# Kernel optimization log

Measured on AMD Instinct MI355X. Metric: run time of the kernel, lower is better.

## Reference

```python
import jax, jax.numpy as jnp
import numpy as np

N = 100000   # nodes
E = 1000000  # directed edges
C = 64       # channels
K = 4        # propagation hops
DT = 1.0     # dt; exp_init=False branch: 2*x + dt^2*conv(x) - x_pre


def setup_inputs() -> dict:
    key = jax.random.key(0)
    k1, k2, k3, k4, k5 = jax.random.split(key, 5)
    x = jax.random.normal(k1, (N, C), dtype=jnp.float32)
    x_pre = jax.random.normal(k2, (N, C), dtype=jnp.float32)
    edge_index = jax.random.randint(k3, (2, E), 0, N, dtype=jnp.int32)
    bound = 1.0 / np.sqrt(C)  # PyG Linear default (kaiming-uniform-like)
    W = jax.random.uniform(k4, (C, C), jnp.float32, -bound, bound)
    b = jax.random.uniform(k5, (C,), jnp.float32, -bound, bound)
    return {"x": x, "x_pre": x_pre, "edge_index": edge_index, "W": W, "b": b}


def _sgc(x, edge_index, W, b):
    # gcn_norm: add self-loops, symmetric normalization D^-1/2 (A+I) D^-1/2
    loop = jnp.arange(N, dtype=edge_index.dtype)
    src = jnp.concatenate([edge_index[0], loop])  # source j
    dst = jnp.concatenate([edge_index[1], loop])  # target i
    deg = jax.ops.segment_sum(jnp.ones(src.shape, jnp.float32), dst, num_segments=N)
    dinv = jnp.where(deg > 0, jax.lax.rsqrt(deg), 0.0)
    norm = dinv[src] * dinv[dst]  # [E+N]
    h = x
    for _ in range(K):  # K-hop sparse propagation (gather -> scale -> scatter-add)
        h = jax.ops.segment_sum(h[src] * norm[:, None], dst, num_segments=N)
    return h @ W.T + b  # SGConv final linear


def reference(x, x_pre, edge_index, W, b):
    return 2.0 * x + (DT * DT) * _sgc(x, edge_index, W, b) - x_pre
```

## Files before the change

### kernel.cpp

```cpp
#include <hip/hip_runtime.h>
#include <hip/hip_fp16.h>

#define CCH 64
#define NBLK 128
#define BKT  256


__global__ void countA(const int* __restrict__ dst, int* __restrict__ cntmat,
                       int E, int chunk, int B) {
    __shared__ int h[512];
    int t = threadIdx.x, blk = blockIdx.x;
    for (int i = t; i < B; i += 256) h[i] = 0;
    __syncthreads();
    int e0 = blk * chunk, e1 = min(e0 + chunk, E);
    for (int e = e0 + t; e < e1; e += 256) atomicAdd(&h[dst[e] >> 8], 1);
    __syncthreads();
    for (int i = t; i < B; i += 256) cntmat[i * NBLK + blk] = h[i];
}

__global__ void scan1(const int* __restrict__ cnt, int* __restrict__ part,
                      int* __restrict__ bsum, int N) {
    __shared__ int s[256];
    int t = threadIdx.x;
    int base = blockIdx.x * 1024 + t * 4;
    int v0 = (base + 0 < N) ? cnt[base + 0] : 0;
    int v1 = (base + 1 < N) ? cnt[base + 1] : 0;
    int v2 = (base + 2 < N) ? cnt[base + 2] : 0;
    int v3 = (base + 3 < N) ? cnt[base + 3] : 0;
    s[t] = v0 + v1 + v2 + v3;
    __syncthreads();
    for (int off = 1; off < 256; off <<= 1) {
        int xx = (t >= off) ? s[t - off] : 0;
        __syncthreads();
        s[t] += xx;
        __syncthreads();
    }
    int excl = (t == 0) ? 0 : s[t - 1];
    if (t == 255) bsum[blockIdx.x] = s[255];
    if (base + 0 < N) part[base + 0] = excl;
    if (base + 1 < N) part[base + 1] = excl + v0;
    if (base + 2 < N) part[base + 2] = excl + v0 + v1;
    if (base + 3 < N) part[base + 3] = excl + v0 + v1 + v2;
}

__global__ void scan2(int* __restrict__ bsum, int NB) {
    __shared__ int s[256];
    int t = threadIdx.x;
    int base = t * 4;
    int v0 = (base + 0 < NB) ? bsum[base + 0] : 0;
    int v1 = (base + 1 < NB) ? bsum[base + 1] : 0;
    int v2 = (base + 2 < NB) ? bsum[base + 2] : 0;
    int v3 = (base + 3 < NB) ? bsum[base + 3] : 0;
    s[t] = v0 + v1 + v2 + v3;
    __syncthreads();
    for (int off = 1; off < 256; off <<= 1) {
        int xx = (t >= off) ? s[t - off] : 0;
        __syncthreads();
        s[t] += xx;
        __syncthreads();
    }
    int excl = (t == 0) ? 0 : s[t - 1];
    if (base + 0 < NB) bsum[base + 0] = excl;
    if (base + 1 < NB) bsum[base + 1] = excl + v0;
    if (base + 2 < NB) bsum[base + 2] = excl + v0 + v1;
    if (base + 3 < NB) bsum[base + 3] = excl + v0 + v1 + v2;
}

__global__ void partA(const int* __restrict__ src, const int* __restrict__ dst,
                      const int* __restrict__ part, const int* __restrict__ bsum,
                      unsigned* __restrict__ brec, int E, int chunk, int B) {
    __shared__ int cur[512];
    int t = threadIdx.x, blk = blockIdx.x;
    for (int i = t; i < B; i += 256) {
        int idx = i * NBLK + blk;
        cur[i] = part[idx] + bsum[idx >> 10];
    }
    __syncthreads();
    int e0 = blk * chunk, e1 = min(e0 + chunk, E);
    for (int e = e0 + t; e < e1; e += 256) {
        int s = src[e], d = dst[e];
        int pos = atomicAdd(&cur[d >> 8], 1);
        brec[pos] = ((unsigned)s << 8) | (unsigned)(d & 255);
    }
}

__global__ void buildB(const unsigned* __restrict__ brec, const int* __restrict__ part,
                       const int* __restrict__ bsum, int* __restrict__ row_ptr,
                       int* __restrict__ adj, float* __restrict__ dinv,
                       float* __restrict__ dinv2, const float* __restrict__ x,
                       __half* __restrict__ xh, int N, int B, int E) {
    __shared__ int hist[256];
    __shared__ int scanbuf[256];
    __shared__ int cursor[256];
    __shared__ float sdinv[256];
    int t = threadIdx.x, k = blockIdx.x;
    int i0 = k * NBLK;
    int base = part[i0] + bsum[i0 >> 10];
    int nextb;
    if (k + 1 < B) {
        int i1 = (k + 1) * NBLK;
        nextb = part[i1] + bsum[i1 >> 10];
    } else {
        nextb = E;
    }
    hist[t] = 0;
    __syncthreads();
    for (int i = base + t; i < nextb; i += 256) atomicAdd(&hist[brec[i] & 255u], 1);
    __syncthreads();
    int v = hist[t];
    scanbuf[t] = v;
    __syncthreads();
    for (int o = 1; o < 256; o <<= 1) {
        int xx = (t >= o) ? scanbuf[t - o] : 0;
        __syncthreads();
        scanbuf[t] += xx;
        __syncthreads();
    }
    int excl = scanbuf[t] - v;
    int node = k * 256 + t;
    float di = 0.f;
    if (node < N) {
        int p = base + excl;
        row_ptr[node] = p;
        cursor[t] = p;
        float dp1 = (float)v + 1.0f;
        di = rsqrtf(dp1);
        dinv[node]  = di;
        dinv2[node] = 1.0f / dp1;
    }
    sdinv[t] = di;
    if (k == 0 && t == 0) row_ptr[N] = E;
    __syncthreads();
    for (int i = base + t; i < nextb; i += 256) {
        unsigned r = brec[i];
        int pos = atomicAdd(&cursor[r & 255u], 1);
        adj[pos] = (int)(r >> 8);
    }
    int nodeBase = k * 256;
    for (int i = t; i < 2048; i += 256) {
        int nl = i >> 3;
        int node2 = nodeBase + nl;
        if (node2 < N) {
            float d = sdinv[nl];
            size_t baseE = (size_t)node2 * 64 + (size_t)(i & 7) * 8;
            float4 a = *(const float4*)&x[baseE];
            float4 c = *(const float4*)&x[baseE + 4];
            float4 o;
            __half2* op = (__half2*)&o;
            op[0] = __float22half2_rn(make_float2(d * a.x, d * a.y));
            op[1] = __float22half2_rn(make_float2(d * a.z, d * a.w));
            op[2] = __float22half2_rn(make_float2(d * c.x, d * c.y));
            op[3] = __float22half2_rn(make_float2(d * c.z, d * c.w));
            *(float4*)&xh[baseE] = o;
        }
    }
}


__device__ __forceinline__ void acc16w(float4 hv, float w, float* acc) {
    __half2* hp = (__half2*)&hv;
    #pragma unroll
    for (int i2 = 0; i2 < 4; ++i2) {
        float2 f = __half22float2(hp[i2]);
        acc[2 * i2]     = fmaf(w, f.x, acc[2 * i2]);
        acc[2 * i2 + 1] = fmaf(w, f.y, acc[2 * i2 + 1]);
    }
}

__global__ void __launch_bounds__(256, 8)
prop_kernel(const __half* __restrict__ hin, __half* __restrict__ hout,
            const int* __restrict__ row_ptr, const int* __restrict__ adj,
            const float* __restrict__ scale, int N, int E) {
    int wid  = (blockIdx.x * blockDim.x + threadIdx.x) >> 6;
    int lane = threadIdx.x & 63;
    int g    = lane >> 3;
    int q    = lane & 7;
    int g8   = g << 3;
    int nb   = wid << 3;
    if (nb >= N) return;
    int node  = nb + g;
    int nodeC = (node < N) ? node : (N - 1);
    int rp0 = row_ptr[nodeC];
    int rp1 = row_ptr[nodeC + 1];
    int cnt = (node < N) ? (rp1 - rp0) : 0;

    int R = cnt;
    R = max(R, __shfl_xor(R, 8, 64));
    R = max(R, __shfl_xor(R, 16, 64));
    R = max(R, __shfl_xor(R, 32, 64));

    const float4* hin16 = (const float4*)hin;

    int eCur = adj[rp0 + q];
    int eNxt = adj[rp0 + 8 + q];

    float4 selfv = hin16[(size_t)nodeC * 8 + q];

    int j0 = __shfl(eCur, g8 + 0, 64); j0 = (0 < cnt) ? j0 : 0;
    int j1 = __shfl(eCur, g8 + 1, 64); j1 = (1 < cnt) ? j1 : 0;
    int j2 = __shfl(eCur, g8 + 2, 64); j2 = (2 < cnt) ? j2 : 0;
    int j3 = __shfl(eCur, g8 + 3, 64); j3 = (3 < cnt) ? j3 : 0;
    float4 gA0 = hin16[(size_t)j0 * 8 + q];
    float4 gA1 = hin16[(size_t)j1 * 8 + q];
    float4 gA2 = hin16[(size_t)j2 * 8 + q];
    float4 gA3 = hin16[(size_t)j3 * 8 + q];
    float4 gB0, gB1, gB2, gB3;

    float acc[8] = {0.f, 0.f, 0.f, 0.f, 0.f, 0.f, 0.f, 0.f};
    acc16w(selfv, 1.f, acc);

    for (int r = 0; r < R; r += 8) {
        int t;
        t = r + 4; j0 = __shfl(eCur, g8 + (t & 7), 64); j0 = (t < cnt) ? j0 : 0;
        t = r + 5; j1 = __shfl(eCur, g8 + (t & 7), 64); j1 = (t < cnt) ? j1 : 0;
        t = r + 6; j2 = __shfl(eCur, g8 + (t & 7), 64); j2 = (t < cnt) ? j2 : 0;
        t = r + 7; j3 = __shfl(eCur, g8 + (t & 7), 64); j3 = (t < cnt) ? j3 : 0;
        gB0 = hin16[(size_t)j0 * 8 + q];
        gB1 = hin16[(size_t)j1 * 8 + q];
        gB2 = hin16[(size_t)j2 * 8 + q];
        gB3 = hin16[(size_t)j3 * 8 + q];
        float w;
        w = (r + 0 < cnt) ? 1.f : 0.f; acc16w(gA0, w, acc);
        w = (r + 1 < cnt) ? 1.f : 0.f; acc16w(gA1, w, acc);
        w = (r + 2 < cnt) ? 1.f : 0.f; acc16w(gA2, w, acc);
        w = (r + 3 < cnt) ? 1.f : 0.f; acc16w(gA3, w, acc);
        t = r + 8;  j0 = __shfl(eNxt, g8 + (t & 7), 64); j0 = (t < cnt) ? j0 : 0;
        t = r + 9;  j1 = __shfl(eNxt, g8 + (t & 7), 64); j1 = (t < cnt) ? j1 : 0;
        t = r + 10; j2 = __shfl(eNxt, g8 + (t & 7), 64); j2 = (t < cnt) ? j2 : 0;
        t = r + 11; j3 = __shfl(eNxt, g8 + (t & 7), 64); j3 = (t < cnt) ? j3 : 0;
        gA0 = hin16[(size_t)j0 * 8 + q];
        gA1 = hin16[(size_t)j1 * 8 + q];
        gA2 = hin16[(size_t)j2 * 8 + q];
        gA3 = hin16[(size_t)j3 * 8 + q];
        w = (r + 4 < cnt) ? 1.f : 0.f; acc16w(gB0, w, acc);
        w = (r + 5 < cnt) ? 1.f : 0.f; acc16w(gB1, w, acc);
        w = (r + 6 < cnt) ? 1.f : 0.f; acc16w(gB2, w, acc);
        w = (r + 7 < cnt) ? 1.f : 0.f; acc16w(gB3, w, acc);
        eCur = eNxt;
        int ao = rp0 + r + 16;
        ao = (ao > E + 96) ? (E + 96) : ao;
        eNxt = adj[ao + q];
    }

    float sc = scale[nodeC];
    if (node < N) {
        float4 o;
        __half2* op = (__half2*)&o;
        op[0] = __float22half2_rn(make_float2(sc * acc[0], sc * acc[1]));
        op[1] = __float22half2_rn(make_float2(sc * acc[2], sc * acc[3]));
        op[2] = __float22half2_rn(make_float2(sc * acc[4], sc * acc[5]));
        op[3] = __float22half2_rn(make_float2(sc * acc[6], sc * acc[7]));
        ((float4*)hout)[(size_t)node * 8 + q] = o;
    }
}

__global__ void __launch_bounds__(256, 2)
final_kernel(const __half* __restrict__ h, const float* __restrict__ x,
             const float* __restrict__ xp, const float* __restrict__ W,
             const float* __restrict__ b, float* __restrict__ out, int N) {
    __shared__ __align__(16) float ht[64 * 68];
    __shared__ __align__(16) float Wt[64 * 68];
    int t = threadIdx.x;
    int nodeBase = blockIdx.x * 64;

    for (int i = t; i < 1024; i += 256) {
        int c  = i >> 4;
        int k4 = i & 15;
        float4 w4 = ((const float4*)W)[i];
        Wt[(k4 * 4 + 0) * 68 + c] = w4.x;
        Wt[(k4 * 4 + 1) * 68 + c] = w4.y;
        Wt[(k4 * 4 + 2) * 68 + c] = w4.z;
        Wt[(k4 * 4 + 3) * 68 + c] = w4.w;
    }
    for (int i = t; i < 512; i += 256) {
        int n  = i >> 3;
        int k8 = i & 7;
        int node = nodeBase + n;
        float4 hv = (node < N) ? ((const float4*)h)[node * 8 + k8]
                               : make_float4(0.f, 0.f, 0.f, 0.f);
        __half2* hp = (__half2*)&hv;
        #pragma unroll
        for (int j = 0; j < 4; ++j) {
            float2 f = __half22float2(hp[j]);
            ht[(k8 * 8 + 2 * j)     * 68 + n] = f.x;
            ht[(k8 * 8 + 2 * j + 1) * 68 + n] = f.y;
        }
    }
    __syncthreads();

    int r0 = (t >> 4) * 4;
    int c0 = (t & 15) * 4;
    float acc[4][4] = {};
    #pragma unroll 8
    for (int k = 0; k < 64; ++k) {
        float4 hv = *(const float4*)&ht[k * 68 + r0];
        float4 wv = *(const float4*)&Wt[k * 68 + c0];
        acc[0][0] = fmaf(hv.x, wv.x, acc[0][0]);
        acc[0][1] = fmaf(hv.x, wv.y, acc[0][1]);
        acc[0][2] = fmaf(hv.x, wv.z, acc[0][2]);
        acc[0][3] = fmaf(hv.x, wv.w, acc[0][3]);
        acc[1][0] = fmaf(hv.y, wv.x, acc[1][0]);
        acc[1][1] = fmaf(hv.y, wv.y, acc[1][1]);
        acc[1][2] = fmaf(hv.y, wv.z, acc[1][2]);
        acc[1][3] = fmaf(hv.y, wv.w, acc[1][3]);
        acc[2][0] = fmaf(hv.z, wv.x, acc[2][0]);
        acc[2][1] = fmaf(hv.z, wv.y, acc[2][1]);
        acc[2][2] = fmaf(hv.z, wv.z, acc[2][2]);
        acc[2][3] = fmaf(hv.z, wv.w, acc[2][3]);
        acc[3][0] = fmaf(hv.w, wv.x, acc[3][0]);
        acc[3][1] = fmaf(hv.w, wv.y, acc[3][1]);
        acc[3][2] = fmaf(hv.w, wv.z, acc[3][2]);
        acc[3][3] = fmaf(hv.w, wv.w, acc[3][3]);
    }

    float4 bv = *(const float4*)&b[c0];
    #pragma unroll
    for (int i = 0; i < 4; ++i) {
        int node = nodeBase + r0 + i;
        if (node >= N) continue;
        int base = node * 64 + c0;
        float4 xv = *(const float4*)&x[base];
        float4 pv = *(const float4*)&xp[base];
        float4 o;
        o.x = fmaf(2.f, xv.x, acc[i][0] + bv.x) - pv.x;
        o.y = fmaf(2.f, xv.y, acc[i][1] + bv.y) - pv.y;
        o.z = fmaf(2.f, xv.z, acc[i][2] + bv.z) - pv.z;
        o.w = fmaf(2.f, xv.w, acc[i][3] + bv.w) - pv.w;
        *(float4*)&out[base] = o;
    }
}

extern "C" void kernel_launch(void* const* d_in, const int* in_sizes, int n_in,
                              void* d_out, int out_size, void* d_ws, size_t ws_size,
                              hipStream_t stream) {
    const float* x    = (const float*)d_in[0];
    const float* xpre = (const float*)d_in[1];
    const int*   ei   = (const int*)d_in[2];
    const float* W    = (const float*)d_in[3];
    const float* b    = (const float*)d_in[4];
    float* out = (float*)d_out;

    const int N = in_sizes[0] / CCH;
    const int E = in_sizes[2] / 2;
    const int* src = ei;
    const int* dst = ei + E;

    const int B     = (N + BKT - 1) / BKT;
    const int M     = B * NBLK;
    const int chunk = (E + NBLK - 1) / NBLK;
    const int NB2   = (M + 1023) / 1024;

    char* p = (char*)d_ws;
    auto alloc = [&](size_t bytes) -> char* {
        char* r = p;
        p += (bytes + 255) & ~(size_t)255;
        return r;
    };
    int*      cntmat  = (int*)alloc((size_t)M * 4);
    int*      part    = (int*)alloc((size_t)M * 4);
    int*      bsum    = (int*)alloc((size_t)NB2 * 4);
    unsigned* brec    = (unsigned*)alloc((size_t)E * 4);
    int*      adj     = (int*)alloc(((size_t)E + 128) * 4);
    int*      row_ptr = (int*)alloc(((size_t)N + 1) * 4);
    float*    dinv    = (float*)alloc((size_t)N * 4);
    float*    dinv2   = (float*)alloc((size_t)N * 4);
    __half*   xh      = (__half*)alloc((size_t)N * CCH * 2);
    __half*   g0      = (__half*)alloc((size_t)N * CCH * 2);
    __half*   g1      = (__half*)alloc((size_t)N * CCH * 2);

    countA<<<NBLK, 256, 0, stream>>>(dst, cntmat, E, chunk, B);
    scan1 <<<NB2, 256, 0, stream>>>(cntmat, part, bsum, M);
    scan2 <<<1, 256, 0, stream>>>(bsum, NB2);
    partA <<<NBLK, 256, 0, stream>>>(src, dst, part, bsum, brec, E, chunk, B);
    buildB<<<B, 256, 0, stream>>>(brec, part, bsum, row_ptr, adj, dinv, dinv2,
                                  x, xh, N, B, E);

    const int nwave = (N + 7) / 8;
    const int pgrid = (nwave + 3) / 4;
    prop_kernel<<<pgrid, 256, 0, stream>>>(xh, g0, row_ptr, adj, dinv2, N, E);
    prop_kernel<<<pgrid, 256, 0, stream>>>(g0, g1, row_ptr, adj, dinv2, N, E);
    prop_kernel<<<pgrid, 256, 0, stream>>>(g1, g0, row_ptr, adj, dinv2, N, E);
    prop_kernel<<<pgrid, 256, 0, stream>>>(g0, g1, row_ptr, adj, dinv,  N, E);

    final_kernel<<<(N + 63) / 64, 256, 0, stream>>>(g1, x, xpre, W, b, out, N);
}
```

Measured before the change: 264.9 us.

## Sort nodes by degree so each wave processes similar-degree nodes

Builds a global in-degree histogram in buildB, scans it, and scatters node ids into a degree-sorted permutation. prop_kernel then maps its 8 nodes per wavefront through that permutation, so the per-wave loop bound (max degree in the group) sits close to each node's real degree and fewer masked gather slots are wasted. The gather loop also skips the B and next-A batches when they fall past the wave's max degree. This adds two small kernels and an extra indirection per node, and it breaks the locality of output writes and self-feature reads, which now follow the permutation instead of node order.

```diff
diff --git a/kernel.cpp b/kernel.cpp
--- a/kernel.cpp
+++ b/kernel.cpp
@@ -4,12 +4,14 @@
 #define CCH 64
 #define NBLK 128
 #define BKT  256
+#define PB   64
 
 
 __global__ void countA(const int* __restrict__ dst, int* __restrict__ cntmat,
-                       int E, int chunk, int B) {
+                       int* __restrict__ ghist, int E, int chunk, int B) {
     __shared__ int h[512];
     int t = threadIdx.x, blk = blockIdx.x;
+    if (blk == 0) ghist[t] = 0;
     for (int i = t; i < B; i += 256) h[i] = 0;
     __syncthreads();
     int e0 = blk * chunk, e1 = min(e0 + chunk, E);
@@ -88,10 +90,12 @@
                        const int* __restrict__ bsum, int* __restrict__ row_ptr,
                        int* __restrict__ adj, float* __restrict__ dinv,
                        float* __restrict__ dinv2, const float* __restrict__ x,
-                       __half* __restrict__ xh, int N, int B, int E) {
+                       __half* __restrict__ xh, int* __restrict__ ghist,
+                       int N, int B, int E) {
     __shared__ int hist[256];
     __shared__ int scanbuf[256];
     __shared__ int cursor[256];
+    __shared__ int dh[256];
     __shared__ float sdinv[256];
     int t = threadIdx.x, k = blockIdx.x;
     int i0 = k * NBLK;
@@ -104,6 +108,7 @@
         nextb = E;
     }
     hist[t] = 0;
+    dh[t] = 0;
     __syncthreads();
     for (int i = base + t; i < nextb; i += 256) atomicAdd(&hist[brec[i] & 255u], 1);
     __syncthreads();
@@ -127,10 +132,12 @@
         di = rsqrtf(dp1);
         dinv[node]  = di;
         dinv2[node] = 1.0f / dp1;
+        atomicAdd(&dh[v < 255 ? v : 255], 1);
     }
     sdinv[t] = di;
     if (k == 0 && t == 0) row_ptr[N] = E;
     __syncthreads();
+    if (dh[t]) atomicAdd(&ghist[t], dh[t]);
     for (int i = base + t; i < nextb; i += 256) {
         unsigned r = brec[i];
         int pos = atomicAdd(&cursor[r & 255u], 1);
@@ -156,6 +163,44 @@
     }
 }
 
+__global__ void permScan(int* __restrict__ h) {
+    __shared__ int s[256];
+    int t = threadIdx.x;
+    int v = h[t];
+    s[t] = v;
+    __syncthreads();
+    for (int o = 1; o < 256; o <<= 1) {
+        int xx = (t >= o) ? s[t - o] : 0;
+        __syncthreads();
+        s[t] += xx;
+        __syncthreads();
+    }
+    h[t] = s[t] - v;
+}
+
+__global__ void permScatter(const int* __restrict__ row_ptr, int* __restrict__ goff,
+                            int* __restrict__ perm, int N, int chunk) {
+    __shared__ int h[256];
+    __shared__ int cur[256];
+    int t = threadIdx.x, blk = blockIdx.x;
+    h[t] = 0;
+    __syncthreads();
+    int n0 = blk * chunk, n1 = min(n0 + chunk, N);
+    for (int n = n0 + t; n < n1; n += 256) {
+        int d = row_ptr[n + 1] - row_ptr[n];
+        atomicAdd(&h[d < 255 ? d : 255], 1);
+    }
+    __syncthreads();
+    if (h[t]) cur[t] = atomicAdd(&goff[t], h[t]);
+    __syncthreads();
+    for (int n = n0 + t; n < n1; n += 256) {
+        int d = row_ptr[n + 1] - row_ptr[n];
+        d = d < 255 ? d : 255;
+        int pos = atomicAdd(&cur[d], 1);
+        perm[pos] = n;
+    }
+}
+
 
 __device__ __forceinline__ void acc16w(float4 hv, float w, float* acc) {
     __half2* hp = (__half2*)&hv;
@@ -170,7 +215,8 @@
 __global__ void __launch_bounds__(256, 8)
 prop_kernel(const __half* __restrict__ hin, __half* __restrict__ hout,
             const int* __restrict__ row_ptr, const int* __restrict__ adj,
-            const float* __restrict__ scale, int N, int E) {
+            const float* __restrict__ scale, const int* __restrict__ perm,
+            int N, int E) {
     int wid  = (blockIdx.x * blockDim.x + threadIdx.x) >> 6;
     int lane = threadIdx.x & 63;
     int g    = lane >> 3;
@@ -178,11 +224,12 @@
     int g8   = g << 3;
     int nb   = wid << 3;
     if (nb >= N) return;
-    int node  = nb + g;
-    int nodeC = (node < N) ? node : (N - 1);
-    int rp0 = row_ptr[nodeC];
-    int rp1 = row_ptr[nodeC + 1];
-    int cnt = (node < N) ? (rp1 - rp0) : 0;
+    int  slot  = nb + g;
+    bool valid = slot < N;
+    int  node  = perm[valid ? slot : 0];
+    int rp0 = row_ptr[node];
+    int rp1 = row_ptr[node + 1];
+    int cnt = valid ? (rp1 - rp0) : 0;
 
     int R = cnt;
     R = max(R, __shfl_xor(R, 8, 64));
@@ -190,60 +237,72 @@
     R = max(R, __shfl_xor(R, 32, 64));
 
     const float4* hin16 = (const float4*)hin;
+    float4 selfv = hin16[(size_t)node * 8 + q];
 
     int eCur = adj[rp0 + q];
-    int eNxt = adj[rp0 + 8 + q];
-
-    float4 selfv = hin16[(size_t)nodeC * 8 + q];
-
-    int j0 = __shfl(eCur, g8 + 0, 64); j0 = (0 < cnt) ? j0 : 0;
-    int j1 = __shfl(eCur, g8 + 1, 64); j1 = (1 < cnt) ? j1 : 0;
-    int j2 = __shfl(eCur, g8 + 2, 64); j2 = (2 < cnt) ? j2 : 0;
-    int j3 = __shfl(eCur, g8 + 3, 64); j3 = (3 < cnt) ? j3 : 0;
-    float4 gA0 = hin16[(size_t)j0 * 8 + q];
-    float4 gA1 = hin16[(size_t)j1 * 8 + q];
-    float4 gA2 = hin16[(size_t)j2 * 8 + q];
-    float4 gA3 = hin16[(size_t)j3 * 8 + q];
-    float4 gB0, gB1, gB2, gB3;
+    int eNxt = 0;
+    float4 gA0, gA1, gA2, gA3, gB0, gB1, gB2, gB3;
+    int j0, j1, j2, j3;
+    if (R > 0) {
+        j0 = __shfl(eCur, g8 + 0, 64); j0 = (0 < cnt) ? j0 : 0;
+        j1 = __shfl(eCur, g8 + 1, 64); j1 = (1 < cnt) ? j1 : 0;
+        j2 = __shfl(eCur, g8 + 2, 64); j2 = (2 < cnt) ? j2 : 0;
+        j3 = __shfl(eCur, g8 + 3, 64); j3 = (3 < cnt) ? j3 : 0;
+        gA0 = hin16[(size_t)j0 * 8 + q];
+        gA1 = hin16[(size_t)j1 * 8 + q];
+        gA2 = hin16[(size_t)j2 * 8 + q];
+        gA3 = hin16[(size_t)j3 * 8 + q];
+        if (R > 8) eNxt = adj[rp0 + 8 + q];
+    }
 
     float acc[8] = {0.f, 0.f, 0.f, 0.f, 0.f, 0.f, 0.f, 0.f};
     acc16w(selfv, 1.f, acc);
 
     for (int r = 0; r < R; r += 8) {
+        bool hb = (r + 4 < R);
+        bool hn = (r + 8 < R);
         int t;
-        t = r + 4; j0 = __shfl(eCur, g8 + (t & 7), 64); j0 = (t < cnt) ? j0 : 0;
-        t = r + 5; j1 = __shfl(eCur, g8 + (t & 7), 64); j1 = (t < cnt) ? j1 : 0;
-        t = r + 6; j2 = __shfl(eCur, g8 + (t & 7), 64); j2 = (t < cnt) ? j2 : 0;
-        t = r + 7; j3 = __shfl(eCur, g8 + (t & 7), 64); j3 = (t < cnt) ? j3 : 0;
-        gB0 = hin16[(size_t)j0 * 8 + q];
-        gB1 = hin16[(size_t)j1 * 8 + q];
-        gB2 = hin16[(size_t)j2 * 8 + q];
-        gB3 = hin16[(size_t)j3 * 8 + q];
+        if (hb) {
+            t = r + 4; j0 = __shfl(eCur, g8 + (t & 7), 64); j0 = (t < cnt) ? j0 : 0;
+            t = r + 5; j1 = __shfl(eCur, g8 + (t & 7), 64); j1 = (t < cnt) ? j1 : 0;
+            t = r + 6; j2 = __shfl(eCur, g8 + (t & 7), 64); j2 = (t < cnt) ? j2 : 0;
+            t = r + 7; j3 = __shfl(eCur, g8 + (t & 7), 64); j3 = (t < cnt) ? j3 : 0;
+            gB0 = hin16[(size_t)j0 * 8 + q];
+            gB1 = hin16[(size_t)j1 * 8 + q];
+            gB2 = hin16[(size_t)j2 * 8 + q];
+            gB3 = hin16[(size_t)j3 * 8 + q];
+        }
         float w;
         w = (r + 0 < cnt) ? 1.f : 0.f; acc16w(gA0, w, acc);
         w = (r + 1 < cnt) ? 1.f : 0.f; acc16w(gA1, w, acc);
         w = (r + 2 < cnt) ? 1.f : 0.f; acc16w(gA2, w, acc);
         w = (r + 3 < cnt) ? 1.f : 0.f; acc16w(gA3, w, acc);
-        t = r + 8;  j0 = __shfl(eNxt, g8 + (t & 7), 64); j0 = (t < cnt) ? j0 : 0;
-        t = r + 9;  j1 = __shfl(eNxt, g8 + (t & 7), 64); j1 = (t < cnt) ? j1 : 0;
-        t = r + 10; j2 = __shfl(eNxt, g8 + (t & 7), 64); j2 = (t < cnt) ? j2 : 0;
-        t = r + 11; j3 = __shfl(eNxt, g8 + (t & 7), 64); j3 = (t < cnt) ? j3 : 0;
-        gA0 = hin16[(size_t)j0 * 8 + q];
-        gA1 = hin16[(size_t)j1 * 8 + q];
-        gA2 = hin16[(size_t)j2 * 8 + q];
-        gA3 = hin16[(size_t)j3 * 8 + q];
-        w = (r + 4 < cnt) ? 1.f : 0.f; acc16w(gB0, w, acc);
-        w = (r + 5 < cnt) ? 1.f : 0.f; acc16w(gB1, w, acc);
-        w = (r + 6 < cnt) ? 1.f : 0.f; acc16w(gB2, w, acc);
-        w = (r + 7 < cnt) ? 1.f : 0.f; acc16w(gB3, w, acc);
-        eCur = eNxt;
-        int ao = rp0 + r + 16;
-        ao = (ao > E + 96) ? (E + 96) : ao;
-        eNxt = adj[ao + q];
-    }
-
-    float sc = scale[nodeC];
-    if (node < N) {
+        if (hn) {
+            t = r + 8;  j0 = __shfl(eNxt, g8 + (t & 7), 64); j0 = (t < cnt) ? j0 : 0;
+            t = r + 9;  j1 = __shfl(eNxt, g8 + (t & 7), 64); j1 = (t < cnt) ? j1 : 0;
+            t = r + 10; j2 = __shfl(eNxt, g8 + (t & 7), 64); j2 = (t < cnt) ? j2 : 0;
+            t = r + 11; j3 = __shfl(eNxt, g8 + (t & 7), 64); j3 = (t < cnt) ? j3 : 0;
+            gA0 = hin16[(size_t)j0 * 8 + q];
+            gA1 = hin16[(size_t)j1 * 8 + q];
+            gA2 = hin16[(size_t)j2 * 8 + q];
+            gA3 = hin16[(size_t)j3 * 8 + q];
+        }
+        if (hb) {
+            w = (r + 4 < cnt) ? 1.f : 0.f; acc16w(gB0, w, acc);
+            w = (r + 5 < cnt) ? 1.f : 0.f; acc16w(gB1, w, acc);
+            w = (r + 6 < cnt) ? 1.f : 0.f; acc16w(gB2, w, acc);
+            w = (r + 7 < cnt) ? 1.f : 0.f; acc16w(gB3, w, acc);
+        }
+        if (hn) {
+            eCur = eNxt;
+            int ao = rp0 + r + 16;
+            ao = (ao > E + 96) ? (E + 96) : ao;
+            eNxt = adj[ao + q];
+        }
+    }
+
+    if (valid) {
+        float sc = scale[node];
         float4 o;
         __half2* op = (__half2*)&o;
         op[0] = __float22half2_rn(make_float2(sc * acc[0], sc * acc[1]));
@@ -349,6 +408,7 @@
     const int M     = B * NBLK;
     const int chunk = (E + NBLK - 1) / NBLK;
     const int NB2   = (M + 1023) / 1024;
+    const int chkP  = (N + PB - 1) / PB;
 
     char* p = (char*)d_ws;
     auto alloc = [&](size_t bytes) -> char* {
@@ -364,23 +424,27 @@
     int*      row_ptr = (int*)alloc(((size_t)N + 1) * 4);
     float*    dinv    = (float*)alloc((size_t)N * 4);
     float*    dinv2   = (float*)alloc((size_t)N * 4);
+    int*      ghist   = (int*)alloc(256 * 4);
+    int*      perm    = (int*)alloc((size_t)N * 4);
     __half*   xh      = (__half*)alloc((size_t)N * CCH * 2);
     __half*   g0      = (__half*)alloc((size_t)N * CCH * 2);
     __half*   g1      = (__half*)alloc((size_t)N * CCH * 2);
 
-    countA<<<NBLK, 256, 0, stream>>>(dst, cntmat, E, chunk, B);
+    countA<<<NBLK, 256, 0, stream>>>(dst, cntmat, ghist, E, chunk, B);
     scan1 <<<NB2, 256, 0, stream>>>(cntmat, part, bsum, M);
     scan2 <<<1, 256, 0, stream>>>(bsum, NB2);
     partA <<<NBLK, 256, 0, stream>>>(src, dst, part, bsum, brec, E, chunk, B);
     buildB<<<B, 256, 0, stream>>>(brec, part, bsum, row_ptr, adj, dinv, dinv2,
-                                  x, xh, N, B, E);
+                                  x, xh, ghist, N, B, E);
+    permScan   <<<1, 256, 0, stream>>>(ghist);
+    permScatter<<<PB, 256, 0, stream>>>(row_ptr, ghist, perm, N, chkP);
 
     const int nwave = (N + 7) / 8;
     const int pgrid = (nwave + 3) / 4;
-    prop_kernel<<<pgrid, 256, 0, stream>>>(xh, g0, row_ptr, adj, dinv2, N, E);
-    prop_kernel<<<pgrid, 256, 0, stream>>>(g0, g1, row_ptr, adj, dinv2, N, E);
-    prop_kernel<<<pgrid, 256, 0, stream>>>(g1, g0, row_ptr, adj, dinv2, N, E);
-    prop_kernel<<<pgrid, 256, 0, stream>>>(g0, g1, row_ptr, adj, dinv,  N, E);
+    prop_kernel<<<pgrid, 256, 0, stream>>>(xh, g0, row_ptr, adj, dinv2, perm, N, E);
+    prop_kernel<<<pgrid, 256, 0, stream>>>(g0, g1, row_ptr, adj, dinv2, perm, N, E);
+    prop_kernel<<<pgrid, 256, 0, stream>>>(g1, g0, row_ptr, adj, dinv2, perm, N, E);
+    prop_kernel<<<pgrid, 256, 0, stream>>>(g0, g1, row_ptr, adj, dinv,  perm, N, E);
 
     final_kernel<<<(N + 63) / 64, 256, 0, stream>>>(g1, x, xpre, W, b, out, N);
 }
```

Result: slower. 438.0 us (+65.3%).

## Fuse last propagation hop with final linear; fold bsum scan into consumers

Applied to the files above, without the earlier changes.

The fourth propagation hop is merged into the final dense-linear kernel. Each block gathers 32 nodes, keeps the scaled fp32 result in shared memory and applies W, b and the 2x - x_pre epilogue directly, so the fp16 intermediate no longer makes a global round trip and one launch is removed. The separate single-block scan2 kernel is also dropped, and partA and buildB each redo the small block-sum scan in shared memory. In exchange, every block reloads and transposes W for only 32 nodes and runs a redundant scan with extra barriers, and the fused kernel's larger shared footprint may lower occupancy during the latency-bound gather.

```diff
diff --git a/kernel.cpp b/kernel.cpp
--- a/kernel.cpp
+++ b/kernel.cpp
@@ -43,37 +43,33 @@
     if (base + 3 < N) part[base + 3] = excl + v0 + v1 + v2;
 }
 
-__global__ void scan2(int* __restrict__ bsum, int NB) {
-    __shared__ int s[256];
-    int t = threadIdx.x;
-    int base = t * 4;
-    int v0 = (base + 0 < NB) ? bsum[base + 0] : 0;
-    int v1 = (base + 1 < NB) ? bsum[base + 1] : 0;
-    int v2 = (base + 2 < NB) ? bsum[base + 2] : 0;
-    int v3 = (base + 3 < NB) ? bsum[base + 3] : 0;
-    s[t] = v0 + v1 + v2 + v3;
-    __syncthreads();
-    for (int off = 1; off < 256; off <<= 1) {
-        int xx = (t >= off) ? s[t - off] : 0;
-        __syncthreads();
-        s[t] += xx;
-        __syncthreads();
-    }
-    int excl = (t == 0) ? 0 : s[t - 1];
-    if (base + 0 < NB) bsum[base + 0] = excl;
-    if (base + 1 < NB) bsum[base + 1] = excl + v0;
-    if (base + 2 < NB) bsum[base + 2] = excl + v0 + v1;
-    if (base + 3 < NB) bsum[base + 3] = excl + v0 + v1 + v2;
+__device__ __forceinline__ void scan_bsum(const int* __restrict__ bsum, int NB2,
+                                          int* sbs, int t) {
+    int v = (t < NB2) ? bsum[t] : 0;
+    sbs[t] = v;
+    __syncthreads();
+    for (int o = 1; o < 256; o <<= 1) {
+        int xx = (t >= o) ? sbs[t - o] : 0;
+        __syncthreads();
+        sbs[t] += xx;
+        __syncthreads();
+    }
+    int e = sbs[t] - v;
+    __syncthreads();
+    sbs[t] = e;
+    __syncthreads();
 }
 
 __global__ void partA(const int* __restrict__ src, const int* __restrict__ dst,
                       const int* __restrict__ part, const int* __restrict__ bsum,
-                      unsigned* __restrict__ brec, int E, int chunk, int B) {
+                      unsigned* __restrict__ brec, int E, int chunk, int B, int NB2) {
     __shared__ int cur[512];
+    __shared__ int sbs[256];
     int t = threadIdx.x, blk = blockIdx.x;
+    scan_bsum(bsum, NB2, sbs, t);
     for (int i = t; i < B; i += 256) {
         int idx = i * NBLK + blk;
-        cur[i] = part[idx] + bsum[idx >> 10];
+        cur[i] = part[idx] + sbs[idx >> 10];
     }
     __syncthreads();
     int e0 = blk * chunk, e1 = min(e0 + chunk, E);
@@ -88,18 +84,20 @@
                        const int* __restrict__ bsum, int* __restrict__ row_ptr,
                        int* __restrict__ adj, float* __restrict__ dinv,
                        float* __restrict__ dinv2, const float* __restrict__ x,
-                       __half* __restrict__ xh, int N, int B, int E) {
+                       __half* __restrict__ xh, int N, int B, int E, int NB2) {
     __shared__ int hist[256];
     __shared__ int scanbuf[256];
     __shared__ int cursor[256];
+    __shared__ int sbs[256];
     __shared__ float sdinv[256];
     int t = threadIdx.x, k = blockIdx.x;
+    scan_bsum(bsum, NB2, sbs, t);
     int i0 = k * NBLK;
-    int base = part[i0] + bsum[i0 >> 10];
+    int base = part[i0] + sbs[i0 >> 10];
     int nextb;
     if (k + 1 < B) {
         int i1 = (k + 1) * NBLK;
-        nextb = part[i1] + bsum[i1 >> 10];
+        nextb = part[i1] + sbs[i1 >> 10];
     } else {
         nextb = E;
     }
@@ -167,22 +165,12 @@
     }
 }
 
-__global__ void __launch_bounds__(256, 8)
-prop_kernel(const __half* __restrict__ hin, __half* __restrict__ hout,
-            const int* __restrict__ row_ptr, const int* __restrict__ adj,
-            const float* __restrict__ scale, int N, int E) {
-    int wid  = (blockIdx.x * blockDim.x + threadIdx.x) >> 6;
-    int lane = threadIdx.x & 63;
-    int g    = lane >> 3;
-    int q    = lane & 7;
-    int g8   = g << 3;
-    int nb   = wid << 3;
-    if (nb >= N) return;
-    int node  = nb + g;
-    int nodeC = (node < N) ? node : (N - 1);
+__device__ __forceinline__ void prop_body(const __half* __restrict__ hin,
+                                          const int* __restrict__ row_ptr,
+                                          const int* __restrict__ adj,
+                                          int nodeC, int cnt, int g8, int q,
+                                          int E, float* acc) {
     int rp0 = row_ptr[nodeC];
-    int rp1 = row_ptr[nodeC + 1];
-    int cnt = (node < N) ? (rp1 - rp0) : 0;
 
     int R = cnt;
     R = max(R, __shfl_xor(R, 8, 64));
@@ -190,12 +178,10 @@
     R = max(R, __shfl_xor(R, 32, 64));
 
     const float4* hin16 = (const float4*)hin;
+    float4 selfv = hin16[(size_t)nodeC * 8 + q];
 
     int eCur = adj[rp0 + q];
     int eNxt = adj[rp0 + 8 + q];
-
-    float4 selfv = hin16[(size_t)nodeC * 8 + q];
-
     int j0 = __shfl(eCur, g8 + 0, 64); j0 = (0 < cnt) ? j0 : 0;
     int j1 = __shfl(eCur, g8 + 1, 64); j1 = (1 < cnt) ? j1 : 0;
     int j2 = __shfl(eCur, g8 + 2, 64); j2 = (2 < cnt) ? j2 : 0;
@@ -206,7 +192,6 @@
     float4 gA3 = hin16[(size_t)j3 * 8 + q];
     float4 gB0, gB1, gB2, gB3;
 
-    float acc[8] = {0.f, 0.f, 0.f, 0.f, 0.f, 0.f, 0.f, 0.f};
     acc16w(selfv, 1.f, acc);
 
     for (int r = 0; r < R; r += 8) {
@@ -241,9 +226,28 @@
         ao = (ao > E + 96) ? (E + 96) : ao;
         eNxt = adj[ao + q];
     }
-
-    float sc = scale[nodeC];
-    if (node < N) {
+}
+
+__global__ void __launch_bounds__(256, 8)
+prop_kernel(const __half* __restrict__ hin, __half* __restrict__ hout,
+            const int* __restrict__ row_ptr, const int* __restrict__ adj,
+            const float* __restrict__ scale, int N, int E) {
+    int wid  = (blockIdx.x * blockDim.x + threadIdx.x) >> 6;
+    int lane = threadIdx.x & 63;
+    int g    = lane >> 3;
+    int q    = lane & 7;
+    int nb   = wid << 3;
+    if (nb >= N) return;
+    int  node  = nb + g;
+    bool valid = node < N;
+    int  nodeC = valid ? node : (N - 1);
+    int cnt = valid ? (row_ptr[nodeC + 1] - row_ptr[nodeC]) : 0;
+
+    float acc[8] = {0.f, 0.f, 0.f, 0.f, 0.f, 0.f, 0.f, 0.f};
+    prop_body(hin, row_ptr, adj, nodeC, cnt, g << 3, q, E, acc);
+
+    if (valid) {
+        float sc = scale[nodeC];
         float4 o;
         __half2* op = (__half2*)&o;
         op[0] = __float22half2_rn(make_float2(sc * acc[0], sc * acc[1]));
@@ -254,14 +258,16 @@
     }
 }
 
-__global__ void __launch_bounds__(256, 2)
-final_kernel(const __half* __restrict__ h, const float* __restrict__ x,
-             const float* __restrict__ xp, const float* __restrict__ W,
-             const float* __restrict__ b, float* __restrict__ out, int N) {
-    __shared__ __align__(16) float ht[64 * 68];
+__global__ void __launch_bounds__(256, 6)
+prop_final_kernel(const __half* __restrict__ hin, const float* __restrict__ x,
+                  const float* __restrict__ xp, const float* __restrict__ W,
+                  const float* __restrict__ b, float* __restrict__ out,
+                  const int* __restrict__ row_ptr, const int* __restrict__ adj,
+                  const float* __restrict__ dinv, int N, int E) {
     __shared__ __align__(16) float Wt[64 * 68];
+    __shared__ __align__(16) float ht[32 * 68];
     int t = threadIdx.x;
-    int nodeBase = blockIdx.x * 64;
+    int nodeBase = blockIdx.x * 32;
 
     for (int i = t; i < 1024; i += 256) {
         int c  = i >> 4;
@@ -272,61 +278,66 @@
         Wt[(k4 * 4 + 2) * 68 + c] = w4.z;
         Wt[(k4 * 4 + 3) * 68 + c] = w4.w;
     }
-    for (int i = t; i < 512; i += 256) {
-        int n  = i >> 3;
-        int k8 = i & 7;
-        int node = nodeBase + n;
-        float4 hv = (node < N) ? ((const float4*)h)[node * 8 + k8]
-                               : make_float4(0.f, 0.f, 0.f, 0.f);
-        __half2* hp = (__half2*)&hv;
-        #pragma unroll
-        for (int j = 0; j < 4; ++j) {
-            float2 f = __half22float2(hp[j]);
-            ht[(k8 * 8 + 2 * j)     * 68 + n] = f.x;
-            ht[(k8 * 8 + 2 * j + 1) * 68 + n] = f.y;
-        }
-    }
-    __syncthreads();
-
-    int r0 = (t >> 4) * 4;
+
+    int wv   = t >> 6;
+    int lane = t & 63;
+    int g    = lane >> 3;
+    int q    = lane & 7;
+    int nl   = wv * 8 + g;
+    int node = nodeBase + nl;
+    bool valid = node < N;
+    int  nodeC = valid ? node : (N - 1);
+    int cnt = valid ? (row_ptr[nodeC + 1] - row_ptr[nodeC]) : 0;
+
+    float acc[8] = {0.f, 0.f, 0.f, 0.f, 0.f, 0.f, 0.f, 0.f};
+    prop_body(hin, row_ptr, adj, nodeC, cnt, g << 3, q, E, acc);
+
+    float sc = valid ? dinv[nodeC] : 0.f;
+    {
+        float* hrow = &ht[nl * 68 + q * 8];
+        float4 h0, h1;
+        h0.x = sc * acc[0]; h0.y = sc * acc[1]; h0.z = sc * acc[2]; h0.w = sc * acc[3];
+        h1.x = sc * acc[4]; h1.y = sc * acc[5]; h1.z = sc * acc[6]; h1.w = sc * acc[7];
+        *(float4*)&hrow[0] = h0;
+        *(float4*)&hrow[4] = h1;
+    }
+    __syncthreads();
+
+    int r0 = t >> 4;
     int c0 = (t & 15) * 4;
-    float acc[4][4] = {};
-    #pragma unroll 8
-    for (int k = 0; k < 64; ++k) {
-        float4 hv = *(const float4*)&ht[k * 68 + r0];
-        float4 wv = *(const float4*)&Wt[k * 68 + c0];
-        acc[0][0] = fmaf(hv.x, wv.x, acc[0][0]);
-        acc[0][1] = fmaf(hv.x, wv.y, acc[0][1]);
-        acc[0][2] = fmaf(hv.x, wv.z, acc[0][2]);
-        acc[0][3] = fmaf(hv.x, wv.w, acc[0][3]);
-        acc[1][0] = fmaf(hv.y, wv.x, acc[1][0]);
-        acc[1][1] = fmaf(hv.y, wv.y, acc[1][1]);
-        acc[1][2] = fmaf(hv.y, wv.z, acc[1][2]);
-        acc[1][3] = fmaf(hv.y, wv.w, acc[1][3]);
-        acc[2][0] = fmaf(hv.z, wv.x, acc[2][0]);
-        acc[2][1] = fmaf(hv.z, wv.y, acc[2][1]);
-        acc[2][2] = fmaf(hv.z, wv.z, acc[2][2]);
-        acc[2][3] = fmaf(hv.z, wv.w, acc[2][3]);
-        acc[3][0] = fmaf(hv.w, wv.x, acc[3][0]);
-        acc[3][1] = fmaf(hv.w, wv.y, acc[3][1]);
-        acc[3][2] = fmaf(hv.w, wv.z, acc[3][2]);
-        acc[3][3] = fmaf(hv.w, wv.w, acc[3][3]);
-    }
-
     float4 bv = *(const float4*)&b[c0];
     #pragma unroll
-    for (int i = 0; i < 4; ++i) {
-        int node = nodeBase + r0 + i;
-        if (node >= N) continue;
-        int base = node * 64 + c0;
-        float4 xv = *(const float4*)&x[base];
-        float4 pv = *(const float4*)&xp[base];
-        float4 o;
-        o.x = fmaf(2.f, xv.x, acc[i][0] + bv.x) - pv.x;
-        o.y = fmaf(2.f, xv.y, acc[i][1] + bv.y) - pv.y;
-        o.z = fmaf(2.f, xv.z, acc[i][2] + bv.z) - pv.z;
-        o.w = fmaf(2.f, xv.w, acc[i][3] + bv.w) - pv.w;
-        *(float4*)&out[base] = o;
+    for (int p = 0; p < 2; ++p) {
+        int n = r0 + p * 16;
+        int nd = nodeBase + n;
+        float4 av = make_float4(0.f, 0.f, 0.f, 0.f);
+        #pragma unroll 4
+        for (int k4 = 0; k4 < 16; ++k4) {
+            float4 h4 = *(const float4*)&ht[n * 68 + k4 * 4];
+            float4 w0 = *(const float4*)&Wt[(k4 * 4 + 0) * 68 + c0];
+            float4 w1 = *(const float4*)&Wt[(k4 * 4 + 1) * 68 + c0];
+            float4 w2 = *(const float4*)&Wt[(k4 * 4 + 2) * 68 + c0];
+            float4 w3 = *(const float4*)&Wt[(k4 * 4 + 3) * 68 + c0];
+            av.x = fmaf(h4.x, w0.x, av.x); av.y = fmaf(h4.x, w0.y, av.y);
+            av.z = fmaf(h4.x, w0.z, av.z); av.w = fmaf(h4.x, w0.w, av.w);
+            av.x = fmaf(h4.y, w1.x, av.x); av.y = fmaf(h4.y, w1.y, av.y);
+            av.z = fmaf(h4.y, w1.z, av.z); av.w = fmaf(h4.y, w1.w, av.w);
+            av.x = fmaf(h4.z, w2.x, av.x); av.y = fmaf(h4.z, w2.y, av.y);
+            av.z = fmaf(h4.z, w2.z, av.z); av.w = fmaf(h4.z, w2.w, av.w);
+            av.x = fmaf(h4.w, w3.x, av.x); av.y = fmaf(h4.w, w3.y, av.y);
+            av.z = fmaf(h4.w, w3.z, av.z); av.w = fmaf(h4.w, w3.w, av.w);
+        }
+        if (nd < N) {
+            int base = nd * 64 + c0;
+            float4 xv = *(const float4*)&x[base];
+            float4 pv = *(const float4*)&xp[base];
+            float4 o;
+            o.x = fmaf(2.f, xv.x, av.x + bv.x) - pv.x;
+            o.y = fmaf(2.f, xv.y, av.y + bv.y) - pv.y;
+            o.z = fmaf(2.f, xv.z, av.z + bv.z) - pv.z;
+            o.w = fmaf(2.f, xv.w, av.w + bv.w) - pv.w;
+            *(float4*)&out[base] = o;
+        }
     }
 }
 
@@ -370,17 +381,16 @@
 
     countA<<<NBLK, 256, 0, stream>>>(dst, cntmat, E, chunk, B);
     scan1 <<<NB2, 256, 0, stream>>>(cntmat, part, bsum, M);
-    scan2 <<<1, 256, 0, stream>>>(bsum, NB2);
-    partA <<<NBLK, 256, 0, stream>>>(src, dst, part, bsum, brec, E, chunk, B);
+    partA <<<NBLK, 256, 0, stream>>>(src, dst, part, bsum, brec, E, chunk, B, NB2);
     buildB<<<B, 256, 0, stream>>>(brec, part, bsum, row_ptr, adj, dinv, dinv2,
-                                  x, xh, N, B, E);
+                                  x, xh, N, B, E, NB2);
 
     const int nwave = (N + 7) / 8;
     const int pgrid = (nwave + 3) / 4;
     prop_kernel<<<pgrid, 256, 0, stream>>>(xh, g0, row_ptr, adj, dinv2, N, E);
     prop_kernel<<<pgrid, 256, 0, stream>>>(g0, g1, row_ptr, adj, dinv2, N, E);
     prop_kernel<<<pgrid, 256, 0, stream>>>(g1, g0, row_ptr, adj, dinv2, N, E);
-    prop_kernel<<<pgrid, 256, 0, stream>>>(g0, g1, row_ptr, adj, dinv,  N, E);
-
-    final_kernel<<<(N + 63) / 64, 256, 0, stream>>>(g1, x, xpre, W, b, out, N);
-}
+    prop_final_kernel<<<(N + 31) / 32, 256, 0, stream>>>(g0, x, xpre, W, b, out,
+                                                         row_ptr, adj, dinv, N, E);
+    (void)g1;
+}
```

Result: faster. 246.8 us (-6.8%).
